# Kernel tuning notes

Measured on AMD Instinct MI355X. Metric: run time of the kernel, lower is better.

The kernel has to match this reference:

```python
import jax, jax.numpy as jnp
import numpy as np

EPS = 1e-5
GROUPS = 8


def setup_inputs() -> dict:
    key = jax.random.key(0)
    ks = jax.random.split(key, 6)
    C = 512
    B, H, W = 4, 64, 64
    s = 1.0 / np.sqrt(C)
    return {
        "x": jax.random.normal(ks[0], (B, C, H, W), dtype=jnp.float32),
        "gn_gamma": jnp.ones((C,), jnp.float32),
        "gn_beta": jnp.zeros((C,), jnp.float32),
        "wq": jax.random.normal(ks[1], (C, C), jnp.float32) * s,
        "bq": jnp.zeros((C,), jnp.float32),
        "wk": jax.random.normal(ks[2], (C, C), jnp.float32) * s,
        "bk": jnp.zeros((C,), jnp.float32),
        "wv": jax.random.normal(ks[3], (C, C), jnp.float32) * s,
        "bv": jnp.zeros((C,), jnp.float32),
        "wp": jax.random.normal(ks[4], (C, C), jnp.float32) * s,
        "bp": jnp.zeros((C,), jnp.float32),
    }


def _group_norm(x, gamma, beta):
    b, c, h, w = x.shape
    xg = x.reshape(b, GROUPS, c // GROUPS, h, w)
    mu = xg.mean(axis=(2, 3, 4), keepdims=True)
    var = xg.var(axis=(2, 3, 4), keepdims=True)
    xn = ((xg - mu) * jax.lax.rsqrt(var + EPS)).reshape(b, c, h, w)
    return xn * gamma[None, :, None, None] + beta[None, :, None, None]


def _conv1x1(x, w, b):
    # 1x1 conv == channel-mixing matmul: [O,C] x [B,C,H,W] -> [B,O,H,W]
    return jnp.einsum('oc,bchw->bohw', w, x) + b[None, :, None, None]


def reference(x, gn_gamma, gn_beta, wq, bq, wk, bk, wv, bv, wp, bp):
    b, c, h, w = x.shape
    xn = _group_norm(x, gn_gamma, gn_beta)  # note: residual uses normalized x, as in source
    q = _conv1x1(xn, wq, bq).reshape(b, c, h * w)
    k = _conv1x1(xn, wk, bk).reshape(b, c, h * w)
    v = _conv1x1(xn, wv, bv).reshape(b, c, h * w)
    scale = jnp.asarray(c, x.dtype) ** 0.5
    attn = jnp.einsum('bci,bcj->bij', q, k) / scale  # [b, hw, hw]
    attn = jax.nn.softmax(attn, axis=2)
    out = jnp.einsum('bij,bcj->bci', attn, v).reshape(b, c, h, w)
    out = _conv1x1(out, wp, bp)
    return xn + out
```

## Files before the change

kernel.cpp:

```cpp
#include <hip/hip_runtime.h>
#include <hip/hip_bf16.h>


typedef unsigned short u16;
typedef unsigned char u8;
typedef __bf16 bf16x8 __attribute__((ext_vector_type(8)));
typedef float f32x4 __attribute__((ext_vector_type(4)));
typedef float f32x16 __attribute__((ext_vector_type(16)));
typedef int i32x4 __attribute__((ext_vector_type(4)));
typedef int i32x8 __attribute__((ext_vector_type(8)));
typedef unsigned short u16x4 __attribute__((ext_vector_type(4)));
typedef unsigned short u16x8 __attribute__((ext_vector_type(8)));

#define CDIM 512
#define NPOS 4096
#define NBATCH 4

__device__ __forceinline__ u16 f2bf(float x) {
  union { float f; unsigned u; } c; c.f = x;
  unsigned u = c.u;
  u += 0x7fffu + ((u >> 16) & 1u);
  return (u16)(u >> 16);
}
__device__ __forceinline__ float bf2f(u16 h) {
  union { unsigned u; float f; } c; c.u = ((unsigned)h) << 16;
  return c.f;
}
__device__ __forceinline__ unsigned pk4_fp8(float a, float b, float c, float d) {
  unsigned v = __builtin_amdgcn_cvt_pk_fp8_f32(a, b, 0, false);
  v = __builtin_amdgcn_cvt_pk_fp8_f32(c, d, v, true);
  return v;
}

__device__ __forceinline__ void async16(const u16* g, u16* l) {
  __builtin_amdgcn_global_load_lds(
      (const __attribute__((address_space(1))) unsigned int*)g,
      (__attribute__((address_space(3))) unsigned int*)l, 16, 0, 0);
}
__device__ __forceinline__ void async16b(const u8* g, u8* l) {
  __builtin_amdgcn_global_load_lds(
      (const __attribute__((address_space(1))) unsigned int*)g,
      (__attribute__((address_space(3))) unsigned int*)l, 16, 0, 0);
}

__device__ __forceinline__ void drain_barrier() {
  asm volatile("s_waitcnt vmcnt(0)" ::: "memory");
  __builtin_amdgcn_s_barrier();
}

__device__ __forceinline__ float wred_sum(float v) {
#pragma unroll
  for (int o = 32; o > 0; o >>= 1) v += __shfl_xor(v, o, 64);
  return v;
}

__global__ __launch_bounds__(256) void gn_partial(const float* __restrict__ x,
                                                  float* __restrict__ stats) {
  int gidx = blockIdx.x >> 3;
  int slice = blockIdx.x & 7;
  const float4* src = (const float4*)x + (long)gidx * 65536 + (long)slice * 8192;
  float s = 0.f, ss = 0.f;
  for (int i = threadIdx.x; i < 8192; i += 256) {
    float4 v = src[i];
    s  += v.x + v.y + v.z + v.w;
    ss += v.x * v.x + v.y * v.y + v.z * v.z + v.w * v.w;
  }
  s = wred_sum(s); ss = wred_sum(ss);
  __shared__ float r1[4], r2[4];
  int lane = threadIdx.x & 63, wave = threadIdx.x >> 6;
  if (lane == 0) { r1[wave] = s; r2[wave] = ss; }
  __syncthreads();
  if (threadIdx.x == 0) {
    atomicAdd(&stats[gidx * 2 + 0], r1[0] + r1[1] + r1[2] + r1[3]);
    atomicAdd(&stats[gidx * 2 + 1], r2[0] + r2[1] + r2[2] + r2[3]);
  }
}

__global__ __launch_bounds__(256) void norm_trans(const float* __restrict__ x,
                                                  const float* __restrict__ stats,
                                                  const float* __restrict__ gamma,
                                                  const float* __restrict__ beta,
                                                  u16* __restrict__ xnb,
                                                  u16* __restrict__ xnT) {
  __shared__ float tile[32][33];
  int b = blockIdx.z, c0 = blockIdx.y * 32, p0 = blockIdx.x * 32;
  int g = (b << 3) + (c0 >> 6);
  float cnt = 1.f / 262144.f;
  float mu = stats[g * 2 + 0] * cnt;
  float ms = stats[g * 2 + 1] * cnt;
  float rstd = rsqrtf(ms - mu * mu + 1e-5f);
  int tp = threadIdx.x & 31, tc = threadIdx.x >> 5;
#pragma unroll
  for (int r = 0; r < 4; r++) {
    int cl = tc + r * 8;
    int c = c0 + cl;
    long idx = ((long)(b * CDIM + c)) * NPOS + p0 + tp;
    float v = (x[idx] - mu) * rstd * gamma[c] + beta[c];
    xnb[idx] = f2bf(v);
    tile[cl][tp] = v;
  }
  __syncthreads();
#pragma unroll
  for (int r = 0; r < 4; r++) {
    int pl = tc + r * 8, cl = tp;
    xnT[((long)(b * NPOS + p0 + pl)) * CDIM + c0 + cl] = f2bf(tile[cl][pl]);
  }
}

__global__ __launch_bounds__(256) void cvt4(const float* __restrict__ a, const float* __restrict__ b,
                                            const float* __restrict__ c, const float* __restrict__ d,
                                            u16* __restrict__ oa, u16* __restrict__ ob,
                                            u16* __restrict__ oc, u16* __restrict__ od) {
  int i = blockIdx.x * 256 + threadIdx.x;
  if (blockIdx.y == 3) {
    int m = i >> 9, k = i & 511;
    u16 v = f2bf(d[i]);
    od[m * 1024 + k] = v;
    od[m * 1024 + 512 + k] = v;
    return;
  }
  const float* src; u16* dst;
  switch (blockIdx.y) {
    case 0: src = a; dst = oa; break;
    case 1: src = b; dst = ob; break;
    default: src = c; dst = oc; break;
  }
  dst[i] = f2bf(src[i]);
}

template <int MODE, int BN>
__global__ __launch_bounds__(BN * 2, 2) void gemm_bt(
    const u16* __restrict__ A, const u16* __restrict__ B,
    void* __restrict__ Cp, const float* __restrict__ bias,
    const float* __restrict__ bias1, const u16* __restrict__ residb,
    const float* __restrict__ laux,
    int N, int K, int lda, int ldb,
    long sA, long sB, long sC, long sR) {
  __shared__ u16 Asm[2][128 * 64];
  __shared__ u16 Bsm[2][BN * 64];
  constexpr int NT = BN * 2;
  constexpr int STEP = NT / 8;
  int bz = blockIdx.z;
  A += (long)bz * sA;
  B += (long)bz * sB;
  int bm = blockIdx.y, bn = blockIdx.x;
  int tid = threadIdx.x;
  int lane = tid & 63, wave = tid >> 6;
  int wm = (wave & 1) * 64, wn = (wave >> 1) * 64;

  int row0 = tid >> 3;
  int ko = (tid & 7) * 8;
  int kos = ko ^ ((row0 & 7) * 8);
  f32x4 acc[4][4] = {};
  int row16 = lane & 15;
  int kq = (lane >> 4) * 8;

  auto stage = [&](int buf, int k0) {
#pragma unroll
    for (int r = 0; r < 128 / STEP; r++) {
      int row = row0 + r * STEP;
      async16(A + (long)(bm * 128 + row) * lda + k0 + kos, &Asm[buf][row * 64 + ko]);
    }
#pragma unroll
    for (int r = 0; r < BN / STEP; r++) {
      int row = row0 + r * STEP;
      async16(B + (long)(bn * BN + row) * ldb + k0 + kos, &Bsm[buf][row * 64 + ko]);
    }
  };

  stage(0, 0);
  drain_barrier();
  int cur = 0;
  for (int k0 = 0; k0 < K; k0 += 64) {
    if (k0 + 64 < K) stage(cur ^ 1, k0 + 64);
#pragma unroll
    for (int s2 = 0; s2 < 2; s2++) {
      bf16x8 af[4], bfr[4];
#pragma unroll
      for (int i = 0; i < 4; i++) {
        int row = wm + i * 16 + row16;
        af[i] = *(const bf16x8*)&Asm[cur][row * 64 + ((s2 * 32 + kq) ^ ((row & 7) * 8))];
      }
#pragma unroll
      for (int j = 0; j < 4; j++) {
        int row = wn + j * 16 + row16;
        bfr[j] = *(const bf16x8*)&Bsm[cur][row * 64 + ((s2 * 32 + kq) ^ ((row & 7) * 8))];
      }
      __builtin_amdgcn_s_setprio(1);
#pragma unroll
      for (int i = 0; i < 4; i++)
#pragma unroll
        for (int j = 0; j < 4; j++)
          acc[i][j] = __builtin_amdgcn_mfma_f32_16x16x32_bf16(bfr[j], af[i], acc[i][j], 0, 0, 0);
      __builtin_amdgcn_s_setprio(0);
    }
    drain_barrier();
    cur ^= 1;
  }

  int mcol = lane & 15, rb = (lane >> 4) * 4;
  long zC = (long)bz * sC;
#pragma unroll
  for (int i = 0; i < 4; i++) {
    int gm = bm * 128 + wm + i * 16 + mcol;
    float bm_add = 0.f;
    if constexpr (MODE == 4 || MODE == 5) bm_add = bias[gm];
#pragma unroll
    for (int j = 0; j < 4; j++) {
      int gn0 = bn * BN + wn + j * 16 + rb;
      long off = zC + (long)gm * N + gn0;
      float v[4];
#pragma unroll
      for (int r = 0; r < 4; r++) v[r] = acc[i][j][r];
      if constexpr (MODE == 0) {
        const float* bb = (gn0 < 512) ? (bias + gn0) : (bias1 + (gn0 - 512));
#pragma unroll
        for (int r = 0; r < 4; r++) v[r] += bb[r];
        *(unsigned*)&((u8*)Cp)[off] = pk4_fp8(v[0], v[1], v[2], v[3]);
      }
      if constexpr (MODE == 4) {
        f32x4 lv = *(const f32x4*)&laux[bz * NPOS + gn0];
        u16x4 rv = *(const u16x4*)&residb[(long)bz * sR + (long)gm * N + gn0];
        f32x4 o;
#pragma unroll
        for (int r = 0; r < 4; r++) o[r] = v[r] / lv[r] + bm_add + bf2f(rv[r]);
        *(f32x4*)&((float*)Cp)[off] = o;
      }
      if constexpr (MODE == 5) {
#pragma unroll
        for (int r = 0; r < 4; r++) v[r] += bm_add;
        *(unsigned*)&((u8*)Cp)[off] = pk4_fp8(v[0], v[1], v[2], v[3]);
      }
    }
  }
}

template <int MODE, int TSTEPS, int LDAB>
__global__ __launch_bounds__(512, 1) void mx_gemm(
    const u8* __restrict__ Abase, const u8* __restrict__ Bbase,
    void* __restrict__ Out, float* __restrict__ l, float scale) {
  __shared__ u8 S[4][2][16384];
  int tid = threadIdx.x, lane = tid & 63, w = tid >> 6;
  int wm = (w & 1) * 128, wn = (w >> 1) * 64;
  int bm = blockIdx.y, bn = blockIdx.x, bz = blockIdx.z;
  int l31 = lane & 31, h = lane >> 5;

  const u8 *Ab, *Bb;
  if constexpr (MODE == 0) {
    Ab = Abase + (long)bz * 4194304;
    Bb = Ab + 512;
  } else {
    int b = bz >> 1, sp = bz & 1;
    Ab = Abase + (long)b * 16777216 + sp * 2048;
    Bb = Bbase + (long)b * 2097152 + sp * 2048;
  }

  f32x16 acc[4][2] = {};

  auto stage = [&](int slot, int k0) {
    u8* dA = &S[slot][0][0];
    u8* dB = &S[slot][1][0];
#pragma unroll
    for (int half = 0; half < 2; half++) {
      int z = tid + half * 512;
      int ldsrow = z >> 3;
      int gch = (z & 7) ^ (ldsrow & 7);
      int row = ldsrow * 2 + (gch >> 2);
      int c16 = gch & 3;
      async16b(Ab + (long)(bm * 256 + row) * LDAB + k0 + c16 * 16, dA + z * 16);
      async16b(Bb + (long)(bn * 256 + row) * LDAB + k0 + c16 * 16, dB + z * 16);
    }
  };

  stage(0, 0);
  stage(1, 64);
  stage(2, 128);

  for (int t = 0; t < TSTEPS; t++) {
    if (t < TSTEPS - 2)      { asm volatile("s_waitcnt vmcnt(8)" ::: "memory"); }
    else if (t == TSTEPS - 2){ asm volatile("s_waitcnt vmcnt(4)" ::: "memory"); }
    else                     { asm volatile("s_waitcnt vmcnt(0)" ::: "memory"); }
    __builtin_amdgcn_s_barrier();
    __builtin_amdgcn_sched_barrier(0);
    if (t + 3 < TSTEPS) stage((t + 3) & 3, (t + 3) * 64);

    int slot = t & 3;
    const u8* As = &S[slot][0][0];
    const u8* Bs = &S[slot][1][0];
    i32x8 af[4], bf[2];
#pragma unroll
    for (int mr = 0; mr < 4; mr++) {
      int r = wm + mr * 32 + l31;
      int lr = r >> 1, sw = lr & 7;
      int g0 = (r & 1) * 4 + h * 2;
      i32x4 lo = *(const i32x4*)&As[lr * 128 + ((g0 ^ sw) * 16)];
      i32x4 hi = *(const i32x4*)&As[lr * 128 + (((g0 + 1) ^ sw) * 16)];
      af[mr] = __builtin_shufflevector(lo, hi, 0, 1, 2, 3, 4, 5, 6, 7);
    }
#pragma unroll
    for (int nr = 0; nr < 2; nr++) {
      int r = wn + nr * 32 + l31;
      int lr = r >> 1, sw = lr & 7;
      int g0 = (r & 1) * 4 + h * 2;
      i32x4 lo = *(const i32x4*)&Bs[lr * 128 + ((g0 ^ sw) * 16)];
      i32x4 hi = *(const i32x4*)&Bs[lr * 128 + (((g0 + 1) ^ sw) * 16)];
      bf[nr] = __builtin_shufflevector(lo, hi, 0, 1, 2, 3, 4, 5, 6, 7);
    }
    __builtin_amdgcn_s_setprio(1);
#pragma unroll
    for (int mr = 0; mr < 4; mr++)
#pragma unroll
      for (int nr = 0; nr < 2; nr++)
        acc[mr][nr] = __builtin_amdgcn_mfma_scale_f32_32x32x64_f8f6f4(
            bf[nr], af[mr], acc[mr][nr], 0, 0, 0, 0x7F7F7F7F, 0, 0x7F7F7F7F);
    __builtin_amdgcn_s_setprio(0);
  }

  if constexpr (MODE == 0) {
    long zC = (long)bz * 16777216;
    u8* P = (u8*)Out;
    float rsum[4] = {0.f, 0.f, 0.f, 0.f};
#pragma unroll
    for (int mr = 0; mr < 4; mr++) {
      int gi = bm * 256 + wm + mr * 32 + l31;
#pragma unroll
      for (int nr = 0; nr < 2; nr++) {
        int jb = bn * 256 + wn + nr * 32 + h * 4;
#pragma unroll
        for (int g = 0; g < 4; g++) {
          float v0 = __expf(acc[mr][nr][g * 4 + 0] * scale);
          float v1 = __expf(acc[mr][nr][g * 4 + 1] * scale);
          float v2 = __expf(acc[mr][nr][g * 4 + 2] * scale);
          float v3 = __expf(acc[mr][nr][g * 4 + 3] * scale);
          rsum[mr] += v0 + v1 + v2 + v3;
          *(unsigned*)&P[zC + (long)gi * 4096 + jb + 8 * g] = pk4_fp8(v0, v1, v2, v3);
        }
      }
    }
#pragma unroll
    for (int mr = 0; mr < 4; mr++) rsum[mr] += __shfl_xor(rsum[mr], 32, 64);
    if (lane < 32) {
      int base = bz * NPOS + bm * 256 + wm + l31;
#pragma unroll
      for (int mr = 0; mr < 4; mr++) atomicAdd(&l[base + mr * 32], rsum[mr]);
    }
  } else {
    int b = bz >> 1, sp = bz & 1;
    long zC = (long)b * 4194304 + sp * 512;
    u16* part = (u16*)Out;
#pragma unroll
    for (int mr = 0; mr < 4; mr++) {
      int gi = bm * 256 + wm + mr * 32 + l31;
#pragma unroll
      for (int nr = 0; nr < 2; nr++) {
        int cb = bn * 256 + wn + nr * 32 + h * 4;
#pragma unroll
        for (int g = 0; g < 4; g++) {
          u16x4 o;
          o[0] = f2bf(acc[mr][nr][g * 4 + 0]);
          o[1] = f2bf(acc[mr][nr][g * 4 + 1]);
          o[2] = f2bf(acc[mr][nr][g * 4 + 2]);
          o[3] = f2bf(acc[mr][nr][g * 4 + 3]);
          *(u16x4*)&part[zC + (long)gi * 1024 + cb + 8 * g] = o;
        }
      }
    }
  }
}

extern "C" void kernel_launch(void* const* d_in, const int* in_sizes, int n_in,
                              void* d_out, int out_size, void* d_ws, size_t ws_size,
                              hipStream_t stream) {
  const float* x     = (const float*)d_in[0];
  const float* gamma = (const float*)d_in[1];
  const float* beta  = (const float*)d_in[2];
  const float* wq = (const float*)d_in[3];
  const float* bq = (const float*)d_in[4];
  const float* wk = (const float*)d_in[5];
  const float* bk = (const float*)d_in[6];
  const float* wv = (const float*)d_in[7];
  const float* bv = (const float*)d_in[8];
  const float* wp = (const float*)d_in[9];
  const float* bp = (const float*)d_in[10];
  float* out = (float*)d_out;

  char* W = (char*)d_ws;
  float* stats = (float*)(W + 0);
  float* l     = (float*)(W + 256);
  u16* xnb  = (u16*)(W + 65792);
  u16* xnT  = (u16*)(W + 16843008);
  u16* wqkb = (u16*)(W + 33620224);
  u16* wvb  = (u16*)(W + 34668800);
  u16* wpd  = (u16*)(W + 35193088);
  u8*  QKf8 = (u8*)(W + 37290240);
  u8*  Vf8  = (u8*)(W + 54067456);
  u16* part = (u16*)(W + 62456064);
  u8*  SP   = (u8*)(W + 96010496);
  (void)in_sizes; (void)n_in; (void)out_size; (void)ws_size;

  hipMemsetAsync(W, 0, 65792, stream);
  gn_partial<<<256, 256, 0, stream>>>(x, stats);
  norm_trans<<<dim3(128, 16, 4), 256, 0, stream>>>(x, stats, gamma, beta, xnb, xnT);
  cvt4<<<dim3(1024, 4), 256, 0, stream>>>(wq, wk, wv, wp, wqkb, wqkb + 262144, wvb, wpd);

  const long NC = (long)NPOS * CDIM;
  const long CN = (long)CDIM * NPOS;
  const float scale = 0.044194173824159216f;

  gemm_bt<0, 128><<<dim3(8, 128, 1), 256, 0, stream>>>(xnT, wqkb, QKf8, bq, bk, nullptr, nullptr,
      1024, CDIM, CDIM, CDIM, 0, 0, 0, 0);
  gemm_bt<5, 128><<<dim3(32, 4, 4), 256, 0, stream>>>(wvb, xnT, Vf8, bv, nullptr, nullptr, nullptr,
      NPOS, CDIM, CDIM, CDIM, 0, NC, CN, 0);
  mx_gemm<0, 8, 1024><<<dim3(16, 16, NBATCH), 512, 0, stream>>>(QKf8, nullptr, SP, l, scale);
  mx_gemm<1, 32, 4096><<<dim3(2, 16, 8), 512, 0, stream>>>(SP, Vf8, part, nullptr, 0.f);
  gemm_bt<4, 128><<<dim3(32, 4, 4), 256, 0, stream>>>(wpd, part, (void*)out, bp, nullptr, xnb, l,
      NPOS, 1024, 1024, 1024, 0, (long)NPOS * 1024, CN, CN);
}
```

Before: 323.3 us.

## Fuse QK^T, exp and PV into a single flash-attention kernel

Replaces the two fp8 GEMM passes, which wrote the full exp-score matrix to global memory and read it back, with one kernel per 64-query tile. Each tile streams K and V blocks through LDS, computes scores with fp8 MFMA, exponentiates into an LDS P buffer and accumulates P·V, with row sums kept in registers. Output is normalized in the epilogue, so the projection GEMM drops the split-K halves, the division by l and the duplicated weight layout. The aim is to remove the large P round trip and the atomics. In exchange the loop has two full barriers per tile, little overlap between loads and compute, and one large-LDS block per CU.

```diff
diff --git a/kernel.cpp b/kernel.cpp
--- a/kernel.cpp
+++ b/kernel.cpp
@@ -10,7 +10,6 @@
 typedef int i32x4 __attribute__((ext_vector_type(4)));
 typedef int i32x8 __attribute__((ext_vector_type(8)));
 typedef unsigned short u16x4 __attribute__((ext_vector_type(4)));
-typedef unsigned short u16x8 __attribute__((ext_vector_type(8)));
 
 #define CDIM 512
 #define NPOS 4096
@@ -112,18 +111,12 @@
                                             u16* __restrict__ oa, u16* __restrict__ ob,
                                             u16* __restrict__ oc, u16* __restrict__ od) {
   int i = blockIdx.x * 256 + threadIdx.x;
-  if (blockIdx.y == 3) {
-    int m = i >> 9, k = i & 511;
-    u16 v = f2bf(d[i]);
-    od[m * 1024 + k] = v;
-    od[m * 1024 + 512 + k] = v;
-    return;
-  }
   const float* src; u16* dst;
   switch (blockIdx.y) {
     case 0: src = a; dst = oa; break;
     case 1: src = b; dst = ob; break;
-    default: src = c; dst = oc; break;
+    case 2: src = c; dst = oc; break;
+    default: src = d; dst = od; break;
   }
   dst[i] = f2bf(src[i]);
 }
@@ -133,7 +126,6 @@
     const u16* __restrict__ A, const u16* __restrict__ B,
     void* __restrict__ Cp, const float* __restrict__ bias,
     const float* __restrict__ bias1, const u16* __restrict__ residb,
-    const float* __restrict__ laux,
     int N, int K, int lda, int ldb,
     long sA, long sB, long sC, long sR) {
   __shared__ u16 Asm[2][128 * 64];
@@ -204,7 +196,7 @@
   for (int i = 0; i < 4; i++) {
     int gm = bm * 128 + wm + i * 16 + mcol;
     float bm_add = 0.f;
-    if constexpr (MODE == 4 || MODE == 5) bm_add = bias[gm];
+    if constexpr (MODE == 5 || MODE == 6) bm_add = bias[gm];
 #pragma unroll
     for (int j = 0; j < 4; j++) {
       int gn0 = bn * BN + wn + j * 16 + rb;
@@ -218,151 +210,150 @@
         for (int r = 0; r < 4; r++) v[r] += bb[r];
         *(unsigned*)&((u8*)Cp)[off] = pk4_fp8(v[0], v[1], v[2], v[3]);
       }
-      if constexpr (MODE == 4) {
-        f32x4 lv = *(const f32x4*)&laux[bz * NPOS + gn0];
+      if constexpr (MODE == 5) {
+#pragma unroll
+        for (int r = 0; r < 4; r++) v[r] += bm_add;
+        *(unsigned*)&((u8*)Cp)[off] = pk4_fp8(v[0], v[1], v[2], v[3]);
+      }
+      if constexpr (MODE == 6) {
         u16x4 rv = *(const u16x4*)&residb[(long)bz * sR + (long)gm * N + gn0];
         f32x4 o;
 #pragma unroll
-        for (int r = 0; r < 4; r++) o[r] = v[r] / lv[r] + bm_add + bf2f(rv[r]);
+        for (int r = 0; r < 4; r++) o[r] = v[r] + bm_add + bf2f(rv[r]);
         *(f32x4*)&((float*)Cp)[off] = o;
       }
-      if constexpr (MODE == 5) {
-#pragma unroll
-        for (int r = 0; r < 4; r++) v[r] += bm_add;
-        *(unsigned*)&((u8*)Cp)[off] = pk4_fp8(v[0], v[1], v[2], v[3]);
-      }
-    }
-  }
-}
-
-template <int MODE, int TSTEPS, int LDAB>
-__global__ __launch_bounds__(512, 1) void mx_gemm(
-    const u8* __restrict__ Abase, const u8* __restrict__ Bbase,
-    void* __restrict__ Out, float* __restrict__ l, float scale) {
-  __shared__ u8 S[4][2][16384];
+    }
+  }
+}
+
+__global__ __launch_bounds__(512, 2) void fattn(const u8* __restrict__ QKf8,
+                                                const u8* __restrict__ Vf8,
+                                                u16* __restrict__ H, float scale) {
+  __shared__ u8 Ksm[65536];
+  __shared__ u8 Vsm[65536];
+  __shared__ u8 Pp[8192];
+  __shared__ float lsum[4][64];
   int tid = threadIdx.x, lane = tid & 63, w = tid >> 6;
-  int wm = (w & 1) * 128, wn = (w >> 1) * 64;
-  int bm = blockIdx.y, bn = blockIdx.x, bz = blockIdx.z;
   int l31 = lane & 31, h = lane >> 5;
-
-  const u8 *Ab, *Bb;
-  if constexpr (MODE == 0) {
-    Ab = Abase + (long)bz * 4194304;
-    Bb = Ab + 512;
-  } else {
-    int b = bz >> 1, sp = bz & 1;
-    Ab = Abase + (long)b * 16777216 + sp * 2048;
-    Bb = Bbase + (long)b * 2097152 + sp * 2048;
-  }
-
-  f32x16 acc[4][2] = {};
-
-  auto stage = [&](int slot, int k0) {
-    u8* dA = &S[slot][0][0];
-    u8* dB = &S[slot][1][0];
-#pragma unroll
-    for (int half = 0; half < 2; half++) {
-      int z = tid + half * 512;
-      int ldsrow = z >> 3;
-      int gch = (z & 7) ^ (ldsrow & 7);
-      int row = ldsrow * 2 + (gch >> 2);
-      int c16 = gch & 3;
-      async16b(Ab + (long)(bm * 256 + row) * LDAB + k0 + c16 * 16, dA + z * 16);
-      async16b(Bb + (long)(bn * 256 + row) * LDAB + k0 + c16 * 16, dB + z * 16);
+  int wi = w >> 2, wj = w & 3;
+  int bm = blockIdx.x, bz = blockIdx.z;
+  const u8* QKb = QKf8 + (long)bz * 4194304;
+  const u8* Vb  = Vf8 + (long)bz * 2097152;
+
+  i32x8 qf[8];
+  {
+    const u8* qrow = QKb + (long)(bm * 64 + wi * 32 + l31) * 1024 + h * 32;
+#pragma unroll
+    for (int s = 0; s < 8; s++) {
+      i32x4 lo = *(const i32x4*)(qrow + s * 64);
+      i32x4 hi = *(const i32x4*)(qrow + s * 64 + 16);
+      qf[s] = __builtin_shufflevector(lo, hi, 0, 1, 2, 3, 4, 5, 6, 7);
+    }
+  }
+
+  auto stageK = [&](int t) {
+#pragma unroll
+    for (int r = 0; r < 8; r++) {
+      int zz = tid + r * 512;
+      int j = zz >> 5, pos = zz & 31;
+      int gch = (pos & 24) | ((pos & 7) ^ (j & 7));
+      async16b(QKb + (long)(t * 128 + j) * 1024 + 512 + gch * 16, &Ksm[zz * 16]);
     }
   };
-
-  stage(0, 0);
-  stage(1, 64);
-  stage(2, 128);
-
-  for (int t = 0; t < TSTEPS; t++) {
-    if (t < TSTEPS - 2)      { asm volatile("s_waitcnt vmcnt(8)" ::: "memory"); }
-    else if (t == TSTEPS - 2){ asm volatile("s_waitcnt vmcnt(4)" ::: "memory"); }
-    else                     { asm volatile("s_waitcnt vmcnt(0)" ::: "memory"); }
-    __builtin_amdgcn_s_barrier();
-    __builtin_amdgcn_sched_barrier(0);
-    if (t + 3 < TSTEPS) stage((t + 3) & 3, (t + 3) * 64);
-
-    int slot = t & 3;
-    const u8* As = &S[slot][0][0];
-    const u8* Bs = &S[slot][1][0];
-    i32x8 af[4], bf[2];
-#pragma unroll
-    for (int mr = 0; mr < 4; mr++) {
-      int r = wm + mr * 32 + l31;
-      int lr = r >> 1, sw = lr & 7;
-      int g0 = (r & 1) * 4 + h * 2;
-      i32x4 lo = *(const i32x4*)&As[lr * 128 + ((g0 ^ sw) * 16)];
-      i32x4 hi = *(const i32x4*)&As[lr * 128 + (((g0 + 1) ^ sw) * 16)];
-      af[mr] = __builtin_shufflevector(lo, hi, 0, 1, 2, 3, 4, 5, 6, 7);
-    }
+  auto stageV = [&](int t) {
+#pragma unroll
+    for (int r = 0; r < 8; r++) {
+      int zz = tid + r * 512;
+      int c = zz >> 3, pos = zz & 7;
+      int gch = pos ^ (c & 7);
+      async16b(Vb + (long)c * 4096 + t * 128 + gch * 16, &Vsm[zz * 16]);
+    }
+  };
+
+  f32x16 acc[2][2] = {};
+  float rsum = 0.f;
+  int i = wi * 32 + l31;
+  int jr = wj * 32 + l31;
+
+  stageK(0);
+
+  for (int t = 0; t < 32; t++) {
+    __syncthreads();
+    stageV(t);
+    f32x16 s16 = {};
+#pragma unroll
+    for (int s = 0; s < 8; s++) {
+      int p0 = 4 * s + 2 * h;
+      int pos0 = (p0 & 24) | ((p0 & 7) ^ (jr & 7));
+      int pos1 = (p0 & 24) | (((p0 + 1) & 7) ^ (jr & 7));
+      i32x4 lo = *(const i32x4*)&Ksm[jr * 512 + pos0 * 16];
+      i32x4 hi = *(const i32x4*)&Ksm[jr * 512 + pos1 * 16];
+      i32x8 bfk = __builtin_shufflevector(lo, hi, 0, 1, 2, 3, 4, 5, 6, 7);
+      __builtin_amdgcn_s_setprio(1);
+      s16 = __builtin_amdgcn_mfma_scale_f32_32x32x64_f8f6f4(
+          bfk, qf[s], s16, 0, 0, 0, 0x7F7F7F7F, 0, 0x7F7F7F7F);
+      __builtin_amdgcn_s_setprio(0);
+    }
+    float pv[16];
+    float rs = 0.f;
+#pragma unroll
+    for (int r = 0; r < 16; r++) { pv[r] = __expf(s16[r] * scale); rs += pv[r]; }
+    rsum += rs + __shfl_xor(rs, 32, 64);
+#pragma unroll
+    for (int g = 0; g < 4; g++) {
+      int ch = wj * 2 + (g >> 1);
+      int pos = ch ^ (i & 7);
+      *(unsigned*)&Pp[i * 128 + pos * 16 + 8 * (g & 1) + 4 * h] =
+          pk4_fp8(pv[4 * g], pv[4 * g + 1], pv[4 * g + 2], pv[4 * g + 3]);
+    }
+    __syncthreads();
+    if (t < 31) stageK(t + 1);
+#pragma unroll
+    for (int kk = 0; kk < 2; kk++) {
+      i32x8 afp[2], bfv[2];
+#pragma unroll
+      for (int mr = 0; mr < 2; mr++) {
+        int ii = mr * 32 + l31;
+        int c0 = kk * 4 + h * 2;
+        i32x4 lo = *(const i32x4*)&Pp[ii * 128 + ((c0) ^ (ii & 7)) * 16];
+        i32x4 hi = *(const i32x4*)&Pp[ii * 128 + ((c0 + 1) ^ (ii & 7)) * 16];
+        afp[mr] = __builtin_shufflevector(lo, hi, 0, 1, 2, 3, 4, 5, 6, 7);
+      }
+#pragma unroll
+      for (int nr = 0; nr < 2; nr++) {
+        int c = w * 64 + nr * 32 + l31;
+        int g0 = kk * 4 + h * 2;
+        i32x4 lo = *(const i32x4*)&Vsm[c * 128 + ((g0) ^ (c & 7)) * 16];
+        i32x4 hi = *(const i32x4*)&Vsm[c * 128 + ((g0 + 1) ^ (c & 7)) * 16];
+        bfv[nr] = __builtin_shufflevector(lo, hi, 0, 1, 2, 3, 4, 5, 6, 7);
+      }
+      __builtin_amdgcn_s_setprio(1);
+#pragma unroll
+      for (int mr = 0; mr < 2; mr++)
+#pragma unroll
+        for (int nr = 0; nr < 2; nr++)
+          acc[mr][nr] = __builtin_amdgcn_mfma_scale_f32_32x32x64_f8f6f4(
+              bfv[nr], afp[mr], acc[mr][nr], 0, 0, 0, 0x7F7F7F7F, 0, 0x7F7F7F7F);
+      __builtin_amdgcn_s_setprio(0);
+    }
+  }
+
+  if (lane < 32) lsum[wj][wi * 32 + l31] = rsum;
+  __syncthreads();
+#pragma unroll
+  for (int mr = 0; mr < 2; mr++) {
+    int li = mr * 32 + l31;
+    float lt = lsum[0][li] + lsum[1][li] + lsum[2][li] + lsum[3][li];
+    float inv = 1.f / lt;
+    long hrow = ((long)bz * NPOS + bm * 64 + li) * 512;
 #pragma unroll
     for (int nr = 0; nr < 2; nr++) {
-      int r = wn + nr * 32 + l31;
-      int lr = r >> 1, sw = lr & 7;
-      int g0 = (r & 1) * 4 + h * 2;
-      i32x4 lo = *(const i32x4*)&Bs[lr * 128 + ((g0 ^ sw) * 16)];
-      i32x4 hi = *(const i32x4*)&Bs[lr * 128 + (((g0 + 1) ^ sw) * 16)];
-      bf[nr] = __builtin_shufflevector(lo, hi, 0, 1, 2, 3, 4, 5, 6, 7);
-    }
-    __builtin_amdgcn_s_setprio(1);
-#pragma unroll
-    for (int mr = 0; mr < 4; mr++)
-#pragma unroll
-      for (int nr = 0; nr < 2; nr++)
-        acc[mr][nr] = __builtin_amdgcn_mfma_scale_f32_32x32x64_f8f6f4(
-            bf[nr], af[mr], acc[mr][nr], 0, 0, 0, 0x7F7F7F7F, 0, 0x7F7F7F7F);
-    __builtin_amdgcn_s_setprio(0);
-  }
-
-  if constexpr (MODE == 0) {
-    long zC = (long)bz * 16777216;
-    u8* P = (u8*)Out;
-    float rsum[4] = {0.f, 0.f, 0.f, 0.f};
-#pragma unroll
-    for (int mr = 0; mr < 4; mr++) {
-      int gi = bm * 256 + wm + mr * 32 + l31;
-#pragma unroll
-      for (int nr = 0; nr < 2; nr++) {
-        int jb = bn * 256 + wn + nr * 32 + h * 4;
-#pragma unroll
-        for (int g = 0; g < 4; g++) {
-          float v0 = __expf(acc[mr][nr][g * 4 + 0] * scale);
-          float v1 = __expf(acc[mr][nr][g * 4 + 1] * scale);
-          float v2 = __expf(acc[mr][nr][g * 4 + 2] * scale);
-          float v3 = __expf(acc[mr][nr][g * 4 + 3] * scale);
-          rsum[mr] += v0 + v1 + v2 + v3;
-          *(unsigned*)&P[zC + (long)gi * 4096 + jb + 8 * g] = pk4_fp8(v0, v1, v2, v3);
-        }
-      }
-    }
-#pragma unroll
-    for (int mr = 0; mr < 4; mr++) rsum[mr] += __shfl_xor(rsum[mr], 32, 64);
-    if (lane < 32) {
-      int base = bz * NPOS + bm * 256 + wm + l31;
-#pragma unroll
-      for (int mr = 0; mr < 4; mr++) atomicAdd(&l[base + mr * 32], rsum[mr]);
-    }
-  } else {
-    int b = bz >> 1, sp = bz & 1;
-    long zC = (long)b * 4194304 + sp * 512;
-    u16* part = (u16*)Out;
-#pragma unroll
-    for (int mr = 0; mr < 4; mr++) {
-      int gi = bm * 256 + wm + mr * 32 + l31;
-#pragma unroll
-      for (int nr = 0; nr < 2; nr++) {
-        int cb = bn * 256 + wn + nr * 32 + h * 4;
-#pragma unroll
-        for (int g = 0; g < 4; g++) {
-          u16x4 o;
-          o[0] = f2bf(acc[mr][nr][g * 4 + 0]);
-          o[1] = f2bf(acc[mr][nr][g * 4 + 1]);
-          o[2] = f2bf(acc[mr][nr][g * 4 + 2]);
-          o[3] = f2bf(acc[mr][nr][g * 4 + 3]);
-          *(u16x4*)&part[zC + (long)gi * 1024 + cb + 8 * g] = o;
-        }
+#pragma unroll
+      for (int g = 0; g < 4; g++) {
+        u16x4 o;
+#pragma unroll
+        for (int r = 0; r < 4; r++) o[r] = f2bf(acc[mr][nr][4 * g + r] * inv);
+        *(u16x4*)&H[hrow + w * 64 + nr * 32 + 8 * g + 4 * h] = o;
       }
     }
   }
@@ -386,33 +377,30 @@
 
   char* W = (char*)d_ws;
   float* stats = (float*)(W + 0);
-  float* l     = (float*)(W + 256);
   u16* xnb  = (u16*)(W + 65792);
   u16* xnT  = (u16*)(W + 16843008);
   u16* wqkb = (u16*)(W + 33620224);
   u16* wvb  = (u16*)(W + 34668800);
-  u16* wpd  = (u16*)(W + 35193088);
+  u16* wpb  = (u16*)(W + 35193088);
   u8*  QKf8 = (u8*)(W + 37290240);
   u8*  Vf8  = (u8*)(W + 54067456);
-  u16* part = (u16*)(W + 62456064);
-  u8*  SP   = (u8*)(W + 96010496);
+  u16* Hws  = (u16*)(W + 62456064);
   (void)in_sizes; (void)n_in; (void)out_size; (void)ws_size;
 
-  hipMemsetAsync(W, 0, 65792, stream);
+  hipMemsetAsync(W, 0, 256, stream);
   gn_partial<<<256, 256, 0, stream>>>(x, stats);
   norm_trans<<<dim3(128, 16, 4), 256, 0, stream>>>(x, stats, gamma, beta, xnb, xnT);
-  cvt4<<<dim3(1024, 4), 256, 0, stream>>>(wq, wk, wv, wp, wqkb, wqkb + 262144, wvb, wpd);
+  cvt4<<<dim3(1024, 4), 256, 0, stream>>>(wq, wk, wv, wp, wqkb, wqkb + 262144, wvb, wpb);
 
   const long NC = (long)NPOS * CDIM;
   const long CN = (long)CDIM * NPOS;
   const float scale = 0.044194173824159216f;
 
-  gemm_bt<0, 128><<<dim3(8, 128, 1), 256, 0, stream>>>(xnT, wqkb, QKf8, bq, bk, nullptr, nullptr,
+  gemm_bt<0, 128><<<dim3(8, 128, 1), 256, 0, stream>>>(xnT, wqkb, QKf8, bq, bk, nullptr,
       1024, CDIM, CDIM, CDIM, 0, 0, 0, 0);
-  gemm_bt<5, 128><<<dim3(32, 4, 4), 256, 0, stream>>>(wvb, xnT, Vf8, bv, nullptr, nullptr, nullptr,
+  gemm_bt<5, 128><<<dim3(32, 4, 4), 256, 0, stream>>>(wvb, xnT, Vf8, bv, nullptr, nullptr,
       NPOS, CDIM, CDIM, CDIM, 0, NC, CN, 0);
-  mx_gemm<0, 8, 1024><<<dim3(16, 16, NBATCH), 512, 0, stream>>>(QKf8, nullptr, SP, l, scale);
-  mx_gemm<1, 32, 4096><<<dim3(2, 16, 8), 512, 0, stream>>>(SP, Vf8, part, nullptr, 0.f);
-  gemm_bt<4, 128><<<dim3(32, 4, 4), 256, 0, stream>>>(wpd, part, (void*)out, bp, nullptr, xnb, l,
-      NPOS, 1024, 1024, 1024, 0, (long)NPOS * 1024, CN, CN);
-}
+  fattn<<<dim3(64, 1, NBATCH), 512, 0, stream>>>(QKf8, Vf8, Hws, scale);
+  gemm_bt<6, 128><<<dim3(32, 4, 4), 256, 0, stream>>>(wpb, Hws, (void*)out, bp, nullptr, xnb,
+      NPOS, CDIM, CDIM, CDIM, 0, (long)NPOS * CDIM, CN, CN);
+}
```

Result: faster. 282.6 us (-12.6%).
